# Kernel tuning notes

Measured on AMD Instinct MI355X. Metric: run time of the kernel, lower is better.

Reference implementation:

```python
import jax, jax.numpy as jnp
import numpy as np

B, T, D, H = 4, 2048, 1024, 16
HD = D // H  # head_dim = 64

def setup_inputs() -> dict:
    key = jax.random.key(0)
    k1, k2, k3 = jax.random.split(key, 3)
    s = 1.0 / np.sqrt(D)
    x = jax.random.normal(k1, (B, T, D), dtype=jnp.float32)
    W_qkv = jax.random.normal(k2, (D, 3 * D), dtype=jnp.float32) * s
    W_proj = jax.random.normal(k3, (D, D), dtype=jnp.float32) * s
    return {"x": x, "W_qkv": W_qkv, "W_proj": W_proj}

def reference(x, W_qkv, W_proj):
    Bq, Tq, C = x.shape
    qkv = x @ W_qkv                                   # [B,T,3C]
    q, k, v = jnp.split(qkv, 3, axis=-1)
    def heads(t):  # [B,T,C] -> [B,H,T,HD]
        return t.reshape(Bq, Tq, H, HD).transpose(0, 2, 1, 3)
    q, k, v = heads(q), heads(k), heads(v)
    scale = 1.0 / np.sqrt(HD)
    att = jnp.einsum('bhqd,bhkd->bhqk', q, k) * scale  # [B,H,T,T]
    causal = jnp.tril(jnp.ones((Tq, Tq), dtype=bool))
    att = jnp.where(causal[None, None], att, -jnp.inf)
    att = jax.nn.softmax(att, axis=-1)
    y = jnp.einsum('bhqk,bhkd->bhqd', att, v)          # [B,H,T,HD]
    y = y.transpose(0, 2, 1, 3).reshape(Bq, Tq, C)
    return y @ W_proj
```

## Files before the change

kernel.cpp:

```cpp
#include <hip/hip_runtime.h>

typedef unsigned short ushort_t;
typedef __attribute__((ext_vector_type(8))) __bf16 bf16x8;
typedef __attribute__((ext_vector_type(4))) float f32x4;
typedef __attribute__((ext_vector_type(16))) float f32x16;
typedef __attribute__((ext_vector_type(4))) float float4v;
typedef __attribute__((ext_vector_type(8))) unsigned short ushort8v;
typedef __attribute__((ext_vector_type(4))) unsigned short ushort4v;
typedef __attribute__((ext_vector_type(4))) unsigned uint4v;

#define T_LEN 2048
#define D_DIM 1024
#define NHEAD 16
#define HDIM 64
#define BH 64
#define MROWS 8192
#define PERQKV ((size_t)BH * T_LEN * HDIM)

__device__ __forceinline__ ushort_t f2bf(float f) {
  unsigned u = __builtin_bit_cast(unsigned, f);
  u = (u + 0x7FFFu + ((u >> 16) & 1u)) >> 16;
  return (ushort_t)u;
}

__device__ __forceinline__ void load_lds16(const ushort_t* g, ushort_t* l) {
  __builtin_amdgcn_global_load_lds((const __attribute__((address_space(1))) void*)g,
                                   (__attribute__((address_space(3))) void*)l, 16, 0, 0);
}

__global__ __launch_bounds__(256) void k_cvt_x(const float* __restrict__ x,
                                               ushort_t* __restrict__ xb) {
  int i = blockIdx.x * 256 + threadIdx.x;
  float4v v = ((const float4v*)x)[i];
  ushort4v o;
  o[0] = f2bf(v[0]); o[1] = f2bf(v[1]); o[2] = f2bf(v[2]); o[3] = f2bf(v[3]);
  ((ushort4v*)xb)[i] = o;
}

__global__ __launch_bounds__(256) void k_transpose(const float* __restrict__ W,
                                                   ushort_t* __restrict__ Wt,
                                                   int R, int C) {
  __shared__ ushort_t tile[32][33];
  int tx = threadIdx.x & 31, ty = threadIdx.x >> 5;
  int r0 = blockIdx.y << 5, c0 = blockIdx.x << 5;
#pragma unroll
  for (int i = 0; i < 4; ++i) {
    int r = ty + i * 8;
    tile[r][tx] = f2bf(W[(size_t)(r0 + r) * C + c0 + tx]);
  }
  __syncthreads();
#pragma unroll
  for (int i = 0; i < 4; ++i) {
    int r = ty + i * 8;
    Wt[(size_t)(c0 + r) * R + r0 + tx] = tile[tx][r];
  }
}

template <int N, int K, int EPI>
__global__ __launch_bounds__(256) void k_gemm(const ushort_t* __restrict__ A,
                                              const ushort_t* __restrict__ Bt,
                                              ushort_t* __restrict__ O16,
                                              float* __restrict__ O32) {
  __shared__ __align__(16) ushort_t Atile[128 * 32];
  __shared__ __align__(16) ushort_t Btile[128 * 32];
  const int tid = threadIdx.x;
  const int lane = tid & 63, w = tid >> 6;
  const int g = lane >> 4, c = lane & 15;
  const int wm = w >> 1, wn = w & 1;
  const int m0 = blockIdx.y * 128, n0 = blockIdx.x * 128;

  f32x4 acc[4][4];
#pragma unroll
  for (int i = 0; i < 4; ++i)
#pragma unroll
    for (int j = 0; j < 4; ++j) acc[i][j] = (f32x4){0.f, 0.f, 0.f, 0.f};

  for (int k0 = 0; k0 < K; k0 += 32) {
    __syncthreads();
#pragma unroll
    for (int r = 0; r < 2; ++r) {
      int flat = r * 256 + tid;
      int row = flat >> 2, slot = flat & 3;
      int gsl = slot ^ (row & 3);
      load_lds16(A + (size_t)(m0 + row) * K + k0 + gsl * 8,
                 &Atile[(r * 256 + w * 64) * 8]);
      load_lds16(Bt + (size_t)(n0 + row) * K + k0 + gsl * 8,
                 &Btile[(r * 256 + w * 64) * 8]);
    }
    __syncthreads();

    bf16x8 af[4], bfr[4];
#pragma unroll
    for (int mi = 0; mi < 4; ++mi) {
      int row = wm * 64 + mi * 16 + c;
      int sl = g ^ (row & 3);
      af[mi] = *(const bf16x8*)&Atile[row * 32 + sl * 8];
    }
#pragma unroll
    for (int ni = 0; ni < 4; ++ni) {
      int row = wn * 64 + ni * 16 + c;
      int sl = g ^ (row & 3);
      bfr[ni] = *(const bf16x8*)&Btile[row * 32 + sl * 8];
    }
#pragma unroll
    for (int mi = 0; mi < 4; ++mi)
#pragma unroll
      for (int ni = 0; ni < 4; ++ni)
        acc[mi][ni] = __builtin_amdgcn_mfma_f32_16x16x32_bf16(af[mi], bfr[ni],
                                                              acc[mi][ni], 0, 0, 0);
  }

#pragma unroll
  for (int mi = 0; mi < 4; ++mi)
#pragma unroll
    for (int ni = 0; ni < 4; ++ni) {
      int n = n0 + wn * 64 + ni * 16 + c;
#pragma unroll
      for (int j = 0; j < 4; ++j) {
        int m = m0 + wm * 64 + mi * 16 + g * 4 + j;
        float v = acc[mi][ni][j];
        if constexpr (EPI == 0) {
          int which = n >> 10, hn = n & 1023;
          int h = hn >> 6, d = hn & 63;
          int b = m >> 11, t = m & 2047;
          if (which == 0) v *= 0.18033688f;
          O16[(size_t)which * PERQKV +
              (((size_t)(b * NHEAD + h) * T_LEN + t) * HDIM + d)] = f2bf(v);
        } else {
          O32[(size_t)m * N + n] = v;
        }
      }
    }
}

__global__ __launch_bounds__(256) void k_attn(const ushort_t* __restrict__ Q,
                                              const ushort_t* __restrict__ Kv,
                                              const ushort_t* __restrict__ Vv,
                                              ushort_t* __restrict__ Y) {
  __shared__ __align__(16) ushort_t Kt[2][64 * 64];
  __shared__ __align__(16) ushort_t Vt[2][64 * 64];

  const int bid = blockIdx.x;
  const int u = bid >> 3;
  const int bh = (bid & 7) * 8 + (u & 7);
  const int v_ = u >> 5, j_ = (u >> 3) & 3;
  const int p = v_ * 4 + ((v_ & 1) ? (3 - j_) : j_);
  const int nkt = 2 * p + 2;

  const int tid = threadIdx.x, lane = tid & 63, w = tid >> 6;
  const int hi = lane >> 5, lc = lane & 31;
  const int q32 = p * 128 + w * 32;
  const size_t base = (size_t)bh * (T_LEN * HDIM);

  bf16x8 qf[4];
#pragma unroll
  for (int st = 0; st < 4; ++st)
    qf[st] = *(const bf16x8*)(Q + base + (size_t)(q32 + lc) * HDIM + st * 16 + hi * 8);

  f32x16 o0, o1;
#pragma unroll
  for (int i = 0; i < 16; ++i) { o0[i] = 0.f; o1[i] = 0.f; }
  float mrun = 0.f, lrun = 0.f;

  const int ksl = tid & 7, krow = tid >> 3;
  const int kpair = tid & 31, vk0 = 2 * kpair, vd0 = (tid >> 5) * 8;

  bf16x8 kreg0, kreg1;
  ushort8v v0r, v1r;
  auto stage_issue = [&](int kt) {
    const ushort_t* kb = Kv + base + (size_t)kt * 64 * HDIM;
    const ushort_t* vb = Vv + base + (size_t)kt * 64 * HDIM;
    v0r = *(const ushort8v*)(vb + (size_t)vk0 * HDIM + vd0);
    v1r = *(const ushort8v*)(vb + (size_t)(vk0 + 1) * HDIM + vd0);
    kreg0 = *(const bf16x8*)(kb + (size_t)krow * HDIM + ksl * 8);
    kreg1 = *(const bf16x8*)(kb + (size_t)(krow + 32) * HDIM + ksl * 8);
  };
  auto stage_write = [&](int buf) {
    *(bf16x8*)&Kt[buf][krow * 64 + ((ksl ^ (krow & 7)) << 3)] = kreg0;
    const int r2 = krow + 32;
    *(bf16x8*)&Kt[buf][r2 * 64 + ((ksl ^ (r2 & 7)) << 3)] = kreg1;
#pragma unroll
    for (int e = 0; e < 8; ++e) {
      int rd = vd0 + e;
      unsigned pv = (unsigned)v0r[e] | ((unsigned)v1r[e] << 16);
      *(unsigned*)&Vt[buf][rd * 64 + (((kpair >> 2) ^ (rd & 7)) << 3) + 2 * (kpair & 3)] = pv;
    }
  };

  stage_issue(0); stage_write(0);
  if (nkt > 1) stage_issue(1);
  __syncthreads();

  for (int kt = 0; kt < nkt; ++kt) {
    const int cur = kt & 1;
    const ushort_t* kbuf = &Kt[cur][0];
    const ushort_t* vbuf = &Vt[cur][0];

    if (kt * 64 <= q32 + 31) {
      f32x16 s0, s1;
#pragma unroll
      for (int i = 0; i < 16; ++i) { s0[i] = 0.f; s1[i] = 0.f; }
#pragma unroll
      for (int st = 0; st < 4; ++st) {
        bf16x8 kf0 = *(const bf16x8*)&kbuf[lc * 64 + (((2 * st + hi) ^ (lc & 7)) << 3)];
        s0 = __builtin_amdgcn_mfma_f32_32x32x16_bf16(kf0, qf[st], s0, 0, 0, 0);
      }
#pragma unroll
      for (int st = 0; st < 4; ++st) {
        bf16x8 kf1 = *(const bf16x8*)&kbuf[(32 + lc) * 64 + (((2 * st + hi) ^ (lc & 7)) << 3)];
        s1 = __builtin_amdgcn_mfma_f32_32x32x16_bf16(kf1, qf[st], s1, 0, 0, 0);
      }

      if (kt * 64 + 63 > q32) {
        const int q = q32 + lc;
#pragma unroll
        for (int r = 0; r < 16; ++r) {
          int cr = (r & 3) + 8 * (r >> 2) + 4 * hi;
          if (kt * 64 + cr > q)      s0[r] = -3.0e38f;
          if (kt * 64 + 32 + cr > q) s1[r] = -3.0e38f;
        }
      }

      float tm[8];
#pragma unroll
      for (int i = 0; i < 8; ++i) tm[i] = fmaxf(fmaxf(s0[i], s0[i + 8]), fmaxf(s1[i], s1[i + 8]));
#pragma unroll
      for (int i = 0; i < 4; ++i) tm[i] = fmaxf(tm[i], tm[i + 4]);
      float tmax = fmaxf(fmaxf(tm[0], tm[1]), fmaxf(tm[2], tm[3]));
      tmax = fmaxf(tmax, __shfl_xor(tmax, 32));

      if (!__all(tmax <= mrun + 11.0f)) {
        float mnew = fmaxf(mrun, tmax);
        float sc = exp2f(mrun - mnew);
        lrun *= sc; mrun = mnew;
#pragma unroll
        for (int r = 0; r < 16; ++r) {
          int cr = (r & 3) + 8 * (r >> 2) + 4 * hi;
          float scr = __shfl(sc, cr);
          o0[r] *= scr; o1[r] *= scr;
        }
      }

#pragma unroll
      for (int r = 0; r < 16; ++r) s0[r] = exp2f(s0[r] - mrun);
#pragma unroll
      for (int r = 0; r < 16; ++r) s1[r] = exp2f(s1[r] - mrun);
      {
        float u0 = 0.f, u1 = 0.f, u2 = 0.f, u3 = 0.f;
#pragma unroll
        for (int i = 0; i < 4; ++i) {
          u0 += s0[i];     u1 += s0[i + 4];  u2 += s0[i + 8];  u3 += s0[i + 12];
          u0 += s1[i];     u1 += s1[i + 4];  u2 += s1[i + 8];  u3 += s1[i + 12];
        }
        lrun += (u0 + u1) + (u2 + u3);
      }

      unsigned wv[16];
#pragma unroll
      for (int i = 0; i < 8; ++i) {
        asm("v_cvt_pk_bf16_f32 %0, %1, %2" : "=v"(wv[i])     : "v"(s0[2 * i]), "v"(s0[2 * i + 1]));
        asm("v_cvt_pk_bf16_f32 %0, %1, %2" : "=v"(wv[8 + i]) : "v"(s1[2 * i]), "v"(s1[2 * i + 1]));
      }
      bf16x8 pf[4];
#pragma unroll
      for (int g4 = 0; g4 < 4; ++g4) {
        unsigned a0 = wv[4 * g4], a1 = wv[4 * g4 + 1];
        unsigned a2 = wv[4 * g4 + 2], a3 = wv[4 * g4 + 3];
        asm("v_permlane32_swap_b32 %0, %1" : "+v"(a0), "+v"(a2));
        asm("v_permlane32_swap_b32 %0, %1" : "+v"(a1), "+v"(a3));
        uint4v fw; fw[0] = a0; fw[1] = a1; fw[2] = a2; fw[3] = a3;
        pf[g4] = __builtin_bit_cast(bf16x8, fw);
      }

#pragma unroll
      for (int km = 0; km < 4; ++km) {
        int gsl = ((2 * km + hi) ^ (lc & 7)) << 3;
        bf16x8 vb0 = *(const bf16x8*)&vbuf[lc * 64 + gsl];
        bf16x8 vb1 = *(const bf16x8*)&vbuf[(32 + lc) * 64 + gsl];
        o0 = __builtin_amdgcn_mfma_f32_32x32x16_bf16(pf[km], vb0, o0, 0, 0, 0);
        o1 = __builtin_amdgcn_mfma_f32_32x32x16_bf16(pf[km], vb1, o1, 0, 0, 0);
      }
    }

    if (kt + 1 < nkt) stage_write((kt + 1) & 1);
    if (kt + 2 < nkt) stage_issue(kt + 2);
    __syncthreads();
  }

  float lt = lrun + __shfl_xor(lrun, 32);
  float invl = 1.f / lt;
  const int b_ = bh >> 4, h_ = bh & 15;
#pragma unroll
  for (int r = 0; r < 16; ++r) {
    int cr = (r & 3) + 8 * (r >> 2) + 4 * hi;
    float iv = __shfl(invl, cr);
    size_t m = (size_t)b_ * T_LEN + q32 + cr;
    Y[m * D_DIM + h_ * HDIM + lc]      = f2bf(o0[r] * iv);
    Y[m * D_DIM + h_ * HDIM + 32 + lc] = f2bf(o1[r] * iv);
  }
}

extern "C" void kernel_launch(void* const* d_in, const int* in_sizes, int n_in,
                              void* d_out, int out_size, void* d_ws, size_t ws_size,
                              hipStream_t stream) {
  const float* x     = (const float*)d_in[0];
  const float* Wqkv  = (const float*)d_in[1];
  const float* Wproj = (const float*)d_in[2];
  float* out = (float*)d_out;
  ushort_t* ws = (ushort_t*)d_ws;

  ushort_t* Xb  = ws;
  ushort_t* WqT = Xb  + (size_t)MROWS * D_DIM;
  ushort_t* WpT = WqT + (size_t)3 * D_DIM * D_DIM;
  ushort_t* Qb  = WpT + (size_t)D_DIM * D_DIM;
  ushort_t* Kb  = Qb + PERQKV;
  ushort_t* Vb  = Kb + PERQKV;
  ushort_t* Yb  = Vb + PERQKV;

  k_cvt_x<<<(MROWS * D_DIM / 4) / 256, 256, 0, stream>>>(x, Xb);
  k_transpose<<<dim3(3 * D_DIM / 32, D_DIM / 32), 256, 0, stream>>>(Wqkv, WqT, D_DIM, 3 * D_DIM);
  k_transpose<<<dim3(D_DIM / 32, D_DIM / 32), 256, 0, stream>>>(Wproj, WpT, D_DIM, D_DIM);
  k_gemm<3 * D_DIM, D_DIM, 0><<<dim3(3 * D_DIM / 128, MROWS / 128), 256, 0, stream>>>(Xb, WqT, Qb, nullptr);
  k_attn<<<1024, 256, 0, stream>>>(Qb, Kb, Vb, Yb);
  k_gemm<D_DIM, D_DIM, 1><<<dim3(D_DIM / 128, MROWS / 128), 256, 0, stream>>>(Yb, WpT, nullptr, out);
}
```

Before: 208.5 us.

## Pair heavy and light causal query tiles per attention block

Each attention block now processes two query tiles of the same head, a long tile (15-i) and a short tile (i), one after the other, so every block does the same amount of causal work. The grid is halved to 512 blocks, and the K/V double-buffer pipeline runs continuously across the tile boundary, with an epilogue and a Q reload in between. This replaces the earlier snake-order scheduling for load balance and removes the tail imbalance, at the cost of fewer blocks and less parallelism on a large GPU.

```diff
diff --git a/kernel.cpp b/kernel.cpp
--- a/kernel.cpp
+++ b/kernel.cpp
@@ -143,15 +143,16 @@
   const int bid = blockIdx.x;
   const int u = bid >> 3;
   const int bh = (bid & 7) * 8 + (u & 7);
-  const int v_ = u >> 5, j_ = (u >> 3) & 3;
-  const int p = v_ * 4 + ((v_ & 1) ? (3 - j_) : j_);
-  const int nkt = 2 * p + 2;
+  const int pairidx = u >> 3;
+  const int pA = 15 - pairidx, pB = pairidx;
+  const int nktA = 2 * pA + 2;
+  const int total = nktA + 2 * pB + 2;
 
   const int tid = threadIdx.x, lane = tid & 63, w = tid >> 6;
   const int hi = lane >> 5, lc = lane & 31;
-  const int q32 = p * 128 + w * 32;
   const size_t base = (size_t)bh * (T_LEN * HDIM);
 
+  int q32 = pA * 128 + w * 32;
   bf16x8 qf[4];
 #pragma unroll
   for (int st = 0; st < 4; ++st)
@@ -187,12 +188,37 @@
     }
   };
 
+  const int b_ = bh >> 4, h_ = bh & 15;
+  auto epilogue = [&]() {
+    float lt = lrun + __shfl_xor(lrun, 32);
+    float invl = 1.f / lt;
+#pragma unroll
+    for (int r = 0; r < 16; ++r) {
+      int cr = (r & 3) + 8 * (r >> 2) + 4 * hi;
+      float iv = __shfl(invl, cr);
+      size_t m = (size_t)b_ * T_LEN + q32 + cr;
+      Y[m * D_DIM + h_ * HDIM + lc]      = f2bf(o0[r] * iv);
+      Y[m * D_DIM + h_ * HDIM + 32 + lc] = f2bf(o1[r] * iv);
+    }
+  };
+
   stage_issue(0); stage_write(0);
-  if (nkt > 1) stage_issue(1);
+  stage_issue(1);
   __syncthreads();
 
-  for (int kt = 0; kt < nkt; ++kt) {
-    const int cur = kt & 1;
+  for (int it = 0; it < total; ++it) {
+    if (it == nktA) {
+      epilogue();
+      q32 = pB * 128 + w * 32;
+#pragma unroll
+      for (int st = 0; st < 4; ++st)
+        qf[st] = *(const bf16x8*)(Q + base + (size_t)(q32 + lc) * HDIM + st * 16 + hi * 8);
+#pragma unroll
+      for (int i = 0; i < 16; ++i) { o0[i] = 0.f; o1[i] = 0.f; }
+      mrun = 0.f; lrun = 0.f;
+    }
+    const int kt = (it < nktA) ? it : it - nktA;
+    const int cur = it & 1;
     const ushort_t* kbuf = &Kt[cur][0];
     const ushort_t* vbuf = &Vt[cur][0];
 
@@ -282,22 +308,15 @@
       }
     }
 
-    if (kt + 1 < nkt) stage_write((kt + 1) & 1);
-    if (kt + 2 < nkt) stage_issue(kt + 2);
+    if (it + 1 < total) stage_write((it + 1) & 1);
+    if (it + 2 < total) {
+      int itn = it + 2;
+      stage_issue((itn < nktA) ? itn : itn - nktA);
+    }
     __syncthreads();
   }
 
-  float lt = lrun + __shfl_xor(lrun, 32);
-  float invl = 1.f / lt;
-  const int b_ = bh >> 4, h_ = bh & 15;
-#pragma unroll
-  for (int r = 0; r < 16; ++r) {
-    int cr = (r & 3) + 8 * (r >> 2) + 4 * hi;
-    float iv = __shfl(invl, cr);
-    size_t m = (size_t)b_ * T_LEN + q32 + cr;
-    Y[m * D_DIM + h_ * HDIM + lc]      = f2bf(o0[r] * iv);
-    Y[m * D_DIM + h_ * HDIM + 32 + lc] = f2bf(o1[r] * iv);
-  }
+  epilogue();
 }
 
 extern "C" void kernel_launch(void* const* d_in, const int* in_sizes, int n_in,
@@ -321,6 +340,6 @@
   k_transpose<<<dim3(3 * D_DIM / 32, D_DIM / 32), 256, 0, stream>>>(Wqkv, WqT, D_DIM, 3 * D_DIM);
   k_transpose<<<dim3(D_DIM / 32, D_DIM / 32), 256, 0, stream>>>(Wproj, WpT, D_DIM, D_DIM);
   k_gemm<3 * D_DIM, D_DIM, 0><<<dim3(3 * D_DIM / 128, MROWS / 128), 256, 0, stream>>>(Xb, WqT, Qb, nullptr);
-  k_attn<<<1024, 256, 0, stream>>>(Qb, Kb, Vb, Yb);
+  k_attn<<<512, 256, 0, stream>>>(Qb, Kb, Vb, Yb);
   k_gemm<D_DIM, D_DIM, 1><<<dim3(D_DIM / 128, MROWS / 128), 256, 0, stream>>>(Yb, WpT, nullptr, out);
 }
```

Measured after the change: 230.7 us. 1.11x slower.

## Split attention into 64-row query tiles with 2-wave blocks and raw v_exp

Applied to the files above, without the earlier changes.

The attention kernel moves from 256-thread blocks covering 128 query rows to 128-thread blocks covering 64 rows, launching 2048 blocks. Blocks are scheduled longest-first (descending p), and the per-tile causal skip branch is dropped because every kv tile now touches both waves. Each thread stages twice as much K/V data per tile. exp2f is replaced with the raw v_exp_f32 instruction. This aims for finer load balance and less wasted work on diagonal tiles, at the cost of more blocks, more redundant K/V loading, and approximate exp without denormal handling.

```diff
diff --git a/kernel.cpp b/kernel.cpp
--- a/kernel.cpp
+++ b/kernel.cpp
@@ -21,6 +21,10 @@
   unsigned u = __builtin_bit_cast(unsigned, f);
   u = (u + 0x7FFFu + ((u >> 16) & 1u)) >> 16;
   return (ushort_t)u;
+}
+
+__device__ __forceinline__ float fast_exp2(float x) {
+  float r; asm("v_exp_f32 %0, %1" : "=v"(r) : "v"(x)); return r;
 }
 
 __device__ __forceinline__ void load_lds16(const ushort_t* g, ushort_t* l) {
@@ -133,7 +137,7 @@
     }
 }
 
-__global__ __launch_bounds__(256) void k_attn(const ushort_t* __restrict__ Q,
+__global__ __launch_bounds__(128) void k_attn(const ushort_t* __restrict__ Q,
                                               const ushort_t* __restrict__ Kv,
                                               const ushort_t* __restrict__ Vv,
                                               ushort_t* __restrict__ Y) {
@@ -141,15 +145,13 @@
   __shared__ __align__(16) ushort_t Vt[2][64 * 64];
 
   const int bid = blockIdx.x;
-  const int u = bid >> 3;
-  const int bh = (bid & 7) * 8 + (u & 7);
-  const int v_ = u >> 5, j_ = (u >> 3) & 3;
-  const int p = v_ * 4 + ((v_ & 1) ? (3 - j_) : j_);
-  const int nkt = 2 * p + 2;
+  const int bh = (bid & 7) * 8 + ((bid >> 3) & 7);
+  const int p = 31 - (bid >> 6);
+  const int nkt = p + 1;
 
   const int tid = threadIdx.x, lane = tid & 63, w = tid >> 6;
   const int hi = lane >> 5, lc = lane & 31;
-  const int q32 = p * 128 + w * 32;
+  const int q32 = p * 64 + w * 32;
   const size_t base = (size_t)bh * (T_LEN * HDIM);
 
   bf16x8 qf[4];
@@ -162,28 +164,36 @@
   for (int i = 0; i < 16; ++i) { o0[i] = 0.f; o1[i] = 0.f; }
   float mrun = 0.f, lrun = 0.f;
 
-  const int ksl = tid & 7, krow = tid >> 3;
+  const int ksl = tid & 7, krow0 = tid >> 3;
   const int kpair = tid & 31, vk0 = 2 * kpair, vd0 = (tid >> 5) * 8;
 
-  bf16x8 kreg0, kreg1;
-  ushort8v v0r, v1r;
+  bf16x8 kreg[4];
+  ushort8v vreg[4];
   auto stage_issue = [&](int kt) {
     const ushort_t* kb = Kv + base + (size_t)kt * 64 * HDIM;
     const ushort_t* vb = Vv + base + (size_t)kt * 64 * HDIM;
-    v0r = *(const ushort8v*)(vb + (size_t)vk0 * HDIM + vd0);
-    v1r = *(const ushort8v*)(vb + (size_t)(vk0 + 1) * HDIM + vd0);
-    kreg0 = *(const bf16x8*)(kb + (size_t)krow * HDIM + ksl * 8);
-    kreg1 = *(const bf16x8*)(kb + (size_t)(krow + 32) * HDIM + ksl * 8);
+    vreg[0] = *(const ushort8v*)(vb + (size_t)vk0 * HDIM + vd0);
+    vreg[1] = *(const ushort8v*)(vb + (size_t)(vk0 + 1) * HDIM + vd0);
+    vreg[2] = *(const ushort8v*)(vb + (size_t)vk0 * HDIM + vd0 + 32);
+    vreg[3] = *(const ushort8v*)(vb + (size_t)(vk0 + 1) * HDIM + vd0 + 32);
+#pragma unroll
+    for (int m = 0; m < 4; ++m)
+      kreg[m] = *(const bf16x8*)(kb + (size_t)(krow0 + 16 * m) * HDIM + ksl * 8);
   };
   auto stage_write = [&](int buf) {
-    *(bf16x8*)&Kt[buf][krow * 64 + ((ksl ^ (krow & 7)) << 3)] = kreg0;
-    const int r2 = krow + 32;
-    *(bf16x8*)&Kt[buf][r2 * 64 + ((ksl ^ (r2 & 7)) << 3)] = kreg1;
+#pragma unroll
+    for (int m = 0; m < 4; ++m) {
+      int r = krow0 + 16 * m;
+      *(bf16x8*)&Kt[buf][r * 64 + ((ksl ^ (r & 7)) << 3)] = kreg[m];
+    }
 #pragma unroll
     for (int e = 0; e < 8; ++e) {
       int rd = vd0 + e;
-      unsigned pv = (unsigned)v0r[e] | ((unsigned)v1r[e] << 16);
+      unsigned pv = (unsigned)vreg[0][e] | ((unsigned)vreg[1][e] << 16);
       *(unsigned*)&Vt[buf][rd * 64 + (((kpair >> 2) ^ (rd & 7)) << 3) + 2 * (kpair & 3)] = pv;
+      int rd2 = rd + 32;
+      unsigned pv2 = (unsigned)vreg[2][e] | ((unsigned)vreg[3][e] << 16);
+      *(unsigned*)&Vt[buf][rd2 * 64 + (((kpair >> 2) ^ (rd2 & 7)) << 3) + 2 * (kpair & 3)] = pv2;
     }
   };
 
@@ -196,90 +206,88 @@
     const ushort_t* kbuf = &Kt[cur][0];
     const ushort_t* vbuf = &Vt[cur][0];
 
-    if (kt * 64 <= q32 + 31) {
-      f32x16 s0, s1;
-#pragma unroll
-      for (int i = 0; i < 16; ++i) { s0[i] = 0.f; s1[i] = 0.f; }
-#pragma unroll
-      for (int st = 0; st < 4; ++st) {
-        bf16x8 kf0 = *(const bf16x8*)&kbuf[lc * 64 + (((2 * st + hi) ^ (lc & 7)) << 3)];
-        s0 = __builtin_amdgcn_mfma_f32_32x32x16_bf16(kf0, qf[st], s0, 0, 0, 0);
+    f32x16 s0, s1;
+#pragma unroll
+    for (int i = 0; i < 16; ++i) { s0[i] = 0.f; s1[i] = 0.f; }
+#pragma unroll
+    for (int st = 0; st < 4; ++st) {
+      bf16x8 kf0 = *(const bf16x8*)&kbuf[lc * 64 + (((2 * st + hi) ^ (lc & 7)) << 3)];
+      s0 = __builtin_amdgcn_mfma_f32_32x32x16_bf16(kf0, qf[st], s0, 0, 0, 0);
+    }
+#pragma unroll
+    for (int st = 0; st < 4; ++st) {
+      bf16x8 kf1 = *(const bf16x8*)&kbuf[(32 + lc) * 64 + (((2 * st + hi) ^ (lc & 7)) << 3)];
+      s1 = __builtin_amdgcn_mfma_f32_32x32x16_bf16(kf1, qf[st], s1, 0, 0, 0);
+    }
+
+    if (kt * 64 + 63 > q32) {
+      const int q = q32 + lc;
+#pragma unroll
+      for (int r = 0; r < 16; ++r) {
+        int cr = (r & 3) + 8 * (r >> 2) + 4 * hi;
+        if (kt * 64 + cr > q)      s0[r] = -3.0e38f;
+        if (kt * 64 + 32 + cr > q) s1[r] = -3.0e38f;
       }
-#pragma unroll
-      for (int st = 0; st < 4; ++st) {
-        bf16x8 kf1 = *(const bf16x8*)&kbuf[(32 + lc) * 64 + (((2 * st + hi) ^ (lc & 7)) << 3)];
-        s1 = __builtin_amdgcn_mfma_f32_32x32x16_bf16(kf1, qf[st], s1, 0, 0, 0);
+    }
+
+    float tm[8];
+#pragma unroll
+    for (int i = 0; i < 8; ++i) tm[i] = fmaxf(fmaxf(s0[i], s0[i + 8]), fmaxf(s1[i], s1[i + 8]));
+#pragma unroll
+    for (int i = 0; i < 4; ++i) tm[i] = fmaxf(tm[i], tm[i + 4]);
+    float tmax = fmaxf(fmaxf(tm[0], tm[1]), fmaxf(tm[2], tm[3]));
+    tmax = fmaxf(tmax, __shfl_xor(tmax, 32));
+
+    if (!__all(tmax <= mrun + 11.0f)) {
+      float mnew = fmaxf(mrun, tmax);
+      float sc = fast_exp2(mrun - mnew);
+      lrun *= sc; mrun = mnew;
+#pragma unroll
+      for (int r = 0; r < 16; ++r) {
+        int cr = (r & 3) + 8 * (r >> 2) + 4 * hi;
+        float scr = __shfl(sc, cr);
+        o0[r] *= scr; o1[r] *= scr;
       }
-
-      if (kt * 64 + 63 > q32) {
-        const int q = q32 + lc;
-#pragma unroll
-        for (int r = 0; r < 16; ++r) {
-          int cr = (r & 3) + 8 * (r >> 2) + 4 * hi;
-          if (kt * 64 + cr > q)      s0[r] = -3.0e38f;
-          if (kt * 64 + 32 + cr > q) s1[r] = -3.0e38f;
-        }
+    }
+
+#pragma unroll
+    for (int r = 0; r < 16; ++r) s0[r] = fast_exp2(s0[r] - mrun);
+#pragma unroll
+    for (int r = 0; r < 16; ++r) s1[r] = fast_exp2(s1[r] - mrun);
+    {
+      float u0 = 0.f, u1 = 0.f, u2 = 0.f, u3 = 0.f;
+#pragma unroll
+      for (int i = 0; i < 4; ++i) {
+        u0 += s0[i];     u1 += s0[i + 4];  u2 += s0[i + 8];  u3 += s0[i + 12];
+        u0 += s1[i];     u1 += s1[i + 4];  u2 += s1[i + 8];  u3 += s1[i + 12];
       }
-
-      float tm[8];
-#pragma unroll
-      for (int i = 0; i < 8; ++i) tm[i] = fmaxf(fmaxf(s0[i], s0[i + 8]), fmaxf(s1[i], s1[i + 8]));
-#pragma unroll
-      for (int i = 0; i < 4; ++i) tm[i] = fmaxf(tm[i], tm[i + 4]);
-      float tmax = fmaxf(fmaxf(tm[0], tm[1]), fmaxf(tm[2], tm[3]));
-      tmax = fmaxf(tmax, __shfl_xor(tmax, 32));
-
-      if (!__all(tmax <= mrun + 11.0f)) {
-        float mnew = fmaxf(mrun, tmax);
-        float sc = exp2f(mrun - mnew);
-        lrun *= sc; mrun = mnew;
-#pragma unroll
-        for (int r = 0; r < 16; ++r) {
-          int cr = (r & 3) + 8 * (r >> 2) + 4 * hi;
-          float scr = __shfl(sc, cr);
-          o0[r] *= scr; o1[r] *= scr;
-        }
-      }
-
-#pragma unroll
-      for (int r = 0; r < 16; ++r) s0[r] = exp2f(s0[r] - mrun);
-#pragma unroll
-      for (int r = 0; r < 16; ++r) s1[r] = exp2f(s1[r] - mrun);
-      {
-        float u0 = 0.f, u1 = 0.f, u2 = 0.f, u3 = 0.f;
-#pragma unroll
-        for (int i = 0; i < 4; ++i) {
-          u0 += s0[i];     u1 += s0[i + 4];  u2 += s0[i + 8];  u3 += s0[i + 12];
-          u0 += s1[i];     u1 += s1[i + 4];  u2 += s1[i + 8];  u3 += s1[i + 12];
-        }
-        lrun += (u0 + u1) + (u2 + u3);
-      }
-
-      unsigned wv[16];
-#pragma unroll
-      for (int i = 0; i < 8; ++i) {
-        asm("v_cvt_pk_bf16_f32 %0, %1, %2" : "=v"(wv[i])     : "v"(s0[2 * i]), "v"(s0[2 * i + 1]));
-        asm("v_cvt_pk_bf16_f32 %0, %1, %2" : "=v"(wv[8 + i]) : "v"(s1[2 * i]), "v"(s1[2 * i + 1]));
-      }
-      bf16x8 pf[4];
-#pragma unroll
-      for (int g4 = 0; g4 < 4; ++g4) {
-        unsigned a0 = wv[4 * g4], a1 = wv[4 * g4 + 1];
-        unsigned a2 = wv[4 * g4 + 2], a3 = wv[4 * g4 + 3];
-        asm("v_permlane32_swap_b32 %0, %1" : "+v"(a0), "+v"(a2));
-        asm("v_permlane32_swap_b32 %0, %1" : "+v"(a1), "+v"(a3));
-        uint4v fw; fw[0] = a0; fw[1] = a1; fw[2] = a2; fw[3] = a3;
-        pf[g4] = __builtin_bit_cast(bf16x8, fw);
-      }
-
-#pragma unroll
-      for (int km = 0; km < 4; ++km) {
-        int gsl = ((2 * km + hi) ^ (lc & 7)) << 3;
-        bf16x8 vb0 = *(const bf16x8*)&vbuf[lc * 64 + gsl];
-        bf16x8 vb1 = *(const bf16x8*)&vbuf[(32 + lc) * 64 + gsl];
-        o0 = __builtin_amdgcn_mfma_f32_32x32x16_bf16(pf[km], vb0, o0, 0, 0, 0);
-        o1 = __builtin_amdgcn_mfma_f32_32x32x16_bf16(pf[km], vb1, o1, 0, 0, 0);
-      }
+      lrun += (u0 + u1) + (u2 + u3);
+    }
+
+    unsigned wv[16];
+#pragma unroll
+    for (int i = 0; i < 8; ++i) {
+      asm("v_cvt_pk_bf16_f32 %0, %1, %2" : "=v"(wv[i])     : "v"(s0[2 * i]), "v"(s0[2 * i + 1]));
+      asm("v_cvt_pk_bf16_f32 %0, %1, %2" : "=v"(wv[8 + i]) : "v"(s1[2 * i]), "v"(s1[2 * i + 1]));
+    }
+    bf16x8 pf[4];
+#pragma unroll
+    for (int g4 = 0; g4 < 4; ++g4) {
+      unsigned a0 = wv[4 * g4], a1 = wv[4 * g4 + 1];
+      unsigned a2 = wv[4 * g4 + 2], a3 = wv[4 * g4 + 3];
+      asm("v_permlane32_swap_b32 %0, %1" : "+v"(a0), "+v"(a2));
+      asm("v_permlane32_swap_b32 %0, %1" : "+v"(a1), "+v"(a3));
+      uint4v fw; fw[0] = a0; fw[1] = a1; fw[2] = a2; fw[3] = a3;
+      pf[g4] = __builtin_bit_cast(bf16x8, fw);
+    }
+
+#pragma unroll
+    for (int km = 0; km < 4; ++km) {
+      int gsl = ((2 * km + hi) ^ (lc & 7)) << 3;
+      bf16x8 vb0 = *(const bf16x8*)&vbuf[lc * 64 + gsl];
+      bf16x8 vb1 = *(const bf16x8*)&vbuf[(32 + lc) * 64 + gsl];
+      o0 = __builtin_amdgcn_mfma_f32_32x32x16_bf16(pf[km], vb0, o0, 0, 0, 0);
+      o1 = __builtin_amdgcn_mfma_f32_32x32x16_bf16(pf[km], vb1, o1, 0, 0, 0);
     }
 
     if (kt + 1 < nkt) stage_write((kt + 1) & 1);
@@ -321,6 +329,6 @@
   k_transpose<<<dim3(3 * D_DIM / 32, D_DIM / 32), 256, 0, stream>>>(Wqkv, WqT, D_DIM, 3 * D_DIM);
   k_transpose<<<dim3(D_DIM / 32, D_DIM / 32), 256, 0, stream>>>(Wproj, WpT, D_DIM, D_DIM);
   k_gemm<3 * D_DIM, D_DIM, 0><<<dim3(3 * D_DIM / 128, MROWS / 128), 256, 0, stream>>>(Xb, WqT, Qb, nullptr);
-  k_attn<<<1024, 256, 0, stream>>>(Qb, Kb, Vb, Yb);
+  k_attn<<<2048, 128, 0, stream>>>(Qb, Kb, Vb, Yb);
   k_gemm<D_DIM, D_DIM, 1><<<dim3(D_DIM / 128, MROWS / 128), 256, 0, stream>>>(Yb, WpT, nullptr, out);
 }
```

Result: faster. 189.6 us (-9.1%).
